# Kernel optimization log

Measured on AMD Instinct MI355X. Metric: run time of the kernel, lower is better.

## Reference

```python
import jax, jax.numpy as jnp
import numpy as np

N_NODES = 100_000
N_EDGES = 1_000_000
H = 128
NUM_STATES = 4
UPPER_T, LOWER_T, NUM_ITERS, TEMP_EVAL = 1.0, 0.1, 10000, 0.1


def temp_by_step(step, upper, lower, num_iters, temp_eval):
    # Python-level schedule: eval temp at step == -1, else linear anneal.
    if step == -1:
        return temp_eval
    frac = min(step / num_iters, 1.0)
    return upper + (lower - upper) * frac


def from_binary_states(states):
    # [*, k] bits -> integer id in [0, 2**k)
    weights = 2 ** jnp.arange(states.shape[-1])
    return (states * weights).sum(-1)


def setup_inputs() -> dict:
    key = jax.random.key(0)
    ks = jax.random.split(key, 20)
    N, E, h = N_NODES, N_EDGES, H
    node_states = jax.random.randint(ks[0], (N, NUM_STATES), 0, 2)
    edge_states = jax.random.randint(ks[1], (E, NUM_STATES), 0, 2)
    scalars = jax.random.normal(ks[2], (E, 1), jnp.float32)
    # first N edges are self-loops ordered by node id (required by the module's
    # node_scalars = scalars[src == dst] indexing convention)
    loops = jnp.arange(N)
    src = jax.random.randint(ks[3], (E - N,), 0, N)
    dst = jax.random.randint(ks[4], (E - N,), 0, N)
    dst = jnp.where(dst == src, (dst + 1) % N, dst)  # no accidental self-loops
    edge_index = jnp.stack([jnp.concatenate([loops, src]),
                            jnp.concatenate([loops, dst])])
    batched_reverse_idx = jax.random.randint(ks[5], (E,), 0, E)
    batch_scalars = jax.random.normal(ks[6], (E, 1, 1), jnp.float32)
    s = 0.02
    params = dict(
        node_emb=s * jax.random.normal(ks[7], (2 ** NUM_STATES, h), jnp.float32),
        edge_emb=s * jax.random.normal(ks[8], (2 ** NUM_STATES, h), jnp.float32),
        combine_W=s * jax.random.normal(ks[9], (2 * h, h), jnp.float32),
        combine_b=jnp.zeros((h,), jnp.float32),
        keep_W=s * jax.random.normal(ks[10], (h, 2), jnp.float32),
        keep_b=jnp.zeros((2,), jnp.float32),
        push_W=s * jax.random.normal(ks[11], (h, 2), jnp.float32),
        push_b=jnp.zeros((2,), jnp.float32),
        push_node_W=s * jax.random.normal(ks[12], (h, 2), jnp.float32),
        push_node_b=jnp.zeros((2,), jnp.float32),
        increment_W=s * jax.random.normal(ks[13], (h, 2), jnp.float32),
        increment_b=jnp.zeros((2,), jnp.float32),
    )
    return dict(node_states=node_states, edge_states=edge_states, scalars=scalars,
                edge_index=edge_index, batched_reverse_idx=batched_reverse_idx,
                batch_scalars=batch_scalars, processor_step=0, training_step=0,
                **params)


def reference(node_states, edge_states, scalars, edge_index, batched_reverse_idx,
              batch_scalars, processor_step, training_step,
              node_emb, edge_emb, combine_W, combine_b, keep_W, keep_b,
              push_W, push_b, push_node_W, push_node_b,
              increment_W, increment_b):
    N = node_states.shape[0]
    tau = temp_by_step(int(training_step), UPPER_T, LOWER_T, NUM_ITERS, TEMP_EVAL)
    # use_noise = config.use_noise (False) and training_step != -1 -> False

    node_fts = node_emb[from_binary_states(node_states)]   # [N, h]
    edge_fts = edge_emb[from_binary_states(edge_states)]   # [E, h]
    src, dst = edge_index[0], edge_index[1]
    fts = jnp.concatenate([edge_fts[batched_reverse_idx], node_fts[src]], axis=1)
    fts = fts @ combine_W + combine_b                       # [E, h]

    s = scalars.reshape(-1)                                 # [E]

    def pair_gumbel_first(W, b):
        # grouped (per-edge pair) softmax; take first component (== [::2])
        logits = (fts @ W + b) / tau                        # [E, 2]
        return jax.nn.softmax(logits, axis=-1)[:, 0]

    increment = 1.0 * pair_gumbel_first(increment_W, increment_b)
    keep = s * pair_gumbel_first(keep_W, keep_b)

    # push: first N edges are self-loops, self-loop of node i is edge i
    push_wo = pair_gumbel_first(push_W, push_b)
    push_w = pair_gumbel_first(push_node_W, push_node_b)
    node_scalars = s[:N]                                    # scalars at self-loops
    s_wo = s - node_scalars[dst]
    s_w = s_wo + node_scalars[src]
    acc = (jax.ops.segment_sum(push_wo * s_wo, dst, num_segments=N)
           + jax.ops.segment_sum(push_w * s_w, dst, num_segments=N))  # [N]
    edge_push = jnp.zeros_like(s).at[:N].set(acc)           # nonzero only on self-loops

    new_scalars = (increment + keep + edge_push)[:, None]   # [E, 1]
    target = batch_scalars[:, processor_step]               # [E, 1]
    loss = jnp.mean((target - new_scalars) ** 2)
    return new_scalars, loss
```

## Files before the change

kernel.cpp:

```cpp
#include <hip/hip_runtime.h>
#include <math.h>

#define N_NODES 100000
#define N_EDGES 1000000
#define HDIM 128
#define N_NONLOOP (N_EDGES - N_NODES)

typedef float  vfloat4 __attribute__((ext_vector_type(4)));

__device__ __forceinline__ float get_invtau(const int* __restrict__ training_step) {
    int step = training_step[0];
    float tau;
    if (step == -1) {
        tau = 0.1f;
    } else {
        float frac = fminf((float)step / 10000.0f, 1.0f);
        tau = 1.0f + (0.1f - 1.0f) * frac;
    }
    return 1.0f / tau;
}

__device__ __forceinline__ float wave_reduce(float v) {
    #pragma unroll
    for (int off = 32; off > 0; off >>= 1) v += __shfl_down(v, off, 64);
    return v;
}

__global__ __launch_bounds__(256) void precompute_tab1(
    const int* __restrict__ node_states,
    const float* __restrict__ s,
    const float* __restrict__ cW,
    const float* __restrict__ kW, const float* __restrict__ pW,
    const float* __restrict__ pnW, const float* __restrict__ iW,
    const int* __restrict__ tstep,
    float2* __restrict__ node_pack,
    float* __restrict__ acc,
    float* __restrict__ loss_out,
    float* __restrict__ uv)
{
    const int n = blockIdx.x * blockDim.x + threadIdx.x;
    if (n < N_NODES) {
        int4 st = ((const int4*)node_states)[n];
        const int idx = st.x + 2 * st.y + 4 * st.z + 8 * st.w;
        float2 np;
        np.x = s[n];
        np.y = __int_as_float(idx);
        node_pack[n] = np;
        acc[n] = 0.f;
    }
    if (n == 0) *loss_out = 0.f;

    if (blockIdx.x < 256) {
        __shared__ float wd[512];
        const float invtau = get_invtau(tstep);
        for (int i = threadIdx.x; i < 512; i += 256) {
            const int h = i >> 7, d = i & 127;
            const float* W = (h == 0) ? kW : (h == 1) ? pW : (h == 2) ? pnW : iW;
            wd[i] = W[2 * d] - W[2 * d + 1];
        }
        __syncthreads();

        const int row  = blockIdx.x * 4 + (threadIdx.x >> 6);
        const int lane = threadIdx.x & 63;
        const int half = row >> 9;
        const int r    = row & 511;
        const int h    = r >> 7, d = r & 127;
        const int cwrow = half * 128 + d;

        float p = cW[cwrow * 128 + lane]      * wd[h * 128 + lane]
                + cW[cwrow * 128 + 64 + lane] * wd[h * 128 + 64 + lane];
        p = wave_reduce(p);
        if (lane == 0) uv[row] = p * invtau;
    }
}

__global__ void tab_stage2(const float* __restrict__ node_emb,
                           const float* __restrict__ edge_emb,
                           const float* __restrict__ cb,
                           const float* __restrict__ kW, const float* __restrict__ kb,
                           const float* __restrict__ pW, const float* __restrict__ pb,
                           const float* __restrict__ pnW, const float* __restrict__ pnb,
                           const float* __restrict__ iW, const float* __restrict__ ib,
                           const int* __restrict__ tstep,
                           const float* __restrict__ uv,
                           float* __restrict__ tabs)
{
    const int w = blockIdx.x * 4 + (threadIdx.x >> 6);
    if (w >= 132) return;
    const int lane = threadIdx.x & 63;
    const float invtau = get_invtau(tstep);

    float p;
    if (w < 128) {
        const int isB = w >> 6, h = (w >> 4) & 3, i = w & 15;
        const float* emb = isB ? node_emb : edge_emb;
        const float* uvp = uv + isB * 512 + h * 128;
        p = emb[i * 128 + lane] * uvp[lane] + emb[i * 128 + 64 + lane] * uvp[64 + lane];
    } else {
        const int h = w - 128;
        const float* W = (h == 0) ? kW : (h == 1) ? pW : (h == 2) ? pnW : iW;
        p = cb[lane]      * (W[2 * lane] - W[2 * lane + 1])
          + cb[64 + lane] * (W[2 * (64 + lane)] - W[2 * (64 + lane) + 1]);
    }
    p = wave_reduce(p);
    if (lane == 0) {
        if (w < 64) {
            const int h = (w >> 4) & 3, i = w & 15;
            tabs[i * 4 + h] = p;
        } else if (w < 128) {
            const int h = (w >> 4) & 3, i = w & 15;
            tabs[64 + i * 4 + h] = p;
        } else {
            const int h = w - 128;
            const float* b = (h == 0) ? kb : (h == 1) ? pb : (h == 2) ? pnb : ib;
            tabs[128 + h] = (p + b[0] - b[1]) * invtau;
        }
    }
}

__global__ __launch_bounds__(256) void edge_kernel(
    const float* __restrict__ s,
    const int* __restrict__ src,
    const int* __restrict__ dst,
    const int* __restrict__ brev,
    const int* __restrict__ edge_states,
    const float2* __restrict__ node_pack,
    const float* __restrict__ tabs,
    const float* __restrict__ target,
    float* __restrict__ acc,
    float* __restrict__ out,
    float* __restrict__ loss_out)
{
    __shared__ float4 sf[33];
    if (threadIdx.x < 33) sf[threadIdx.x] = ((const float4*)tabs)[threadIdx.x];
    __syncthreads();

    const int t = blockIdx.x * blockDim.x + threadIdx.x;
    float lsum = 0.f;

    if (t < N_NONLOOP / 4) {
        const int g = (N_NODES / 4) + t;
        const int4   rv = ((const int4*)brev)[g];
        const int4   sr = ((const int4*)src)[g];
        const int4   ds = ((const int4*)dst)[g];
        const float4 sv = ((const float4*)s)[g];
        const vfloat4 tg = __builtin_nontemporal_load(&((const vfloat4*)target)[g]);

        const int rvv[4] = {rv.x, rv.y, rv.z, rv.w};
        const int srv[4] = {sr.x, sr.y, sr.z, sr.w};
        const int dsv[4] = {ds.x, ds.y, ds.z, ds.w};
        const float svv[4] = {sv.x, sv.y, sv.z, sv.w};
        const float tgv[4] = {tg.x, tg.y, tg.z, tg.w};

        int4  es[4];
        float2 np[4];
        float sd[4];
        #pragma unroll
        for (int j = 0; j < 4; ++j) {
            es[j] = ((const int4*)edge_states)[rvv[j]];
            np[j] = node_pack[srv[j]];
            sd[j] = node_pack[dsv[j]].x;
        }

        const float4 c4 = sf[32];
        float ov[4];
        #pragma unroll
        for (int j = 0; j < 4; ++j) {
            const int ei = es[j].x + 2 * es[j].y + 4 * es[j].z + 8 * es[j].w;
            const int   ni = __float_as_int(np[j].y);
            const float ss = np[j].x;
            const float4 a = sf[ei];
            const float4 b = sf[16 + ni];
            const float lk  = a.x + b.x + c4.x;
            const float lp  = a.y + b.y + c4.y;
            const float lpn = a.z + b.z + c4.z;
            const float li  = a.w + b.w + c4.w;
            const float pk  = 1.f / (1.f + __expf(-lk));
            const float pp  = 1.f / (1.f + __expf(-lp));
            const float ppn = 1.f / (1.f + __expf(-lpn));
            const float pi  = 1.f / (1.f + __expf(-li));

            const float s_wo = svv[j] - sd[j];
            const float s_w  = s_wo + ss;
            unsafeAtomicAdd(&acc[dsv[j]], pp * s_wo + ppn * s_w);

            ov[j] = pi + svv[j] * pk;
            const float d = tgv[j] - ov[j];
            lsum += d * d;
        }
        vfloat4 o4 = {ov[0], ov[1], ov[2], ov[3]};
        __builtin_nontemporal_store(o4, &((vfloat4*)out)[g]);
    }

    lsum = wave_reduce(lsum);
    __shared__ float wsum[4];
    const int lane = threadIdx.x & 63, wid = threadIdx.x >> 6;
    if (lane == 0) wsum[wid] = lsum;
    __syncthreads();
    if (threadIdx.x == 0) {
        const float tot = wsum[0] + wsum[1] + wsum[2] + wsum[3];
        atomicAdd(loss_out, tot * (1.0f / (float)N_EDGES));
    }
}

__global__ __launch_bounds__(256) void finalize_nodes(
    const int* __restrict__ brev,
    const int* __restrict__ edge_states,
    const float2* __restrict__ node_pack,
    const float* __restrict__ tabs,
    const float* __restrict__ target,
    const float* __restrict__ acc,
    float* __restrict__ out,
    float* __restrict__ loss_out)
{
    __shared__ float4 sf[33];
    if (threadIdx.x < 33) sf[threadIdx.x] = ((const float4*)tabs)[threadIdx.x];
    __syncthreads();

    const int n = blockIdx.x * blockDim.x + threadIdx.x;
    float sq = 0.f;
    if (n < N_NODES) {
        const int    rev = brev[n];
        const int4   est = ((const int4*)edge_states)[rev];
        const int    ei  = est.x + 2 * est.y + 4 * est.z + 8 * est.w;
        const float2 np  = node_pack[n];
        const int    ni  = __float_as_int(np.y);
        const float  sv  = np.x;

        const float4 a = sf[ei];
        const float4 b = sf[16 + ni];
        const float4 c4 = sf[32];
        const float lk  = a.x + b.x + c4.x;
        const float lpn = a.z + b.z + c4.z;
        const float li  = a.w + b.w + c4.w;
        const float pk  = 1.f / (1.f + __expf(-lk));
        const float ppn = 1.f / (1.f + __expf(-lpn));
        const float pi  = 1.f / (1.f + __expf(-li));

        const float v = pi + sv * (pk + ppn) + acc[n];
        out[n] = v;
        const float d = target[n] - v;
        sq = d * d;
    }
    sq = wave_reduce(sq);
    __shared__ float wsum[4];
    const int lane = threadIdx.x & 63, wid = threadIdx.x >> 6;
    if (lane == 0) wsum[wid] = sq;
    __syncthreads();
    if (threadIdx.x == 0) {
        const float tot = wsum[0] + wsum[1] + wsum[2] + wsum[3];
        atomicAdd(loss_out, tot * (1.0f / (float)N_EDGES));
    }
}

extern "C" void kernel_launch(void* const* d_in, const int* in_sizes, int n_in,
                              void* d_out, int out_size, void* d_ws, size_t ws_size,
                              hipStream_t stream) {
    const int*   node_states   = (const int*)d_in[0];
    const int*   edge_states   = (const int*)d_in[1];
    const float* scalars       = (const float*)d_in[2];
    const int*   edge_index    = (const int*)d_in[3];
    const int*   brev          = (const int*)d_in[4];
    const float* batch_scalars = (const float*)d_in[5];
    const int*   training_step = (const int*)d_in[7];
    const float* node_emb  = (const float*)d_in[8];
    const float* edge_emb  = (const float*)d_in[9];
    const float* combine_W = (const float*)d_in[10];
    const float* combine_b = (const float*)d_in[11];
    const float* keep_W  = (const float*)d_in[12];
    const float* keep_b  = (const float*)d_in[13];
    const float* push_W  = (const float*)d_in[14];
    const float* push_b  = (const float*)d_in[15];
    const float* pushn_W = (const float*)d_in[16];
    const float* pushn_b = (const float*)d_in[17];
    const float* inc_W   = (const float*)d_in[18];
    const float* inc_b   = (const float*)d_in[19];

    float* out = (float*)d_out;

    char* ws = (char*)d_ws;
    float*  tabs = (float*)ws;
    float*  uv   = (float*)(ws + 1024);
    float*  acc  = (float*)(ws + 1024 + 4096);
    float2* node_pack = (float2*)(ws + 1024 + 4096 + (size_t)N_NODES * 4);

    const int* srcp = edge_index;
    const int* dstp = edge_index + N_EDGES;

    precompute_tab1<<<(N_NODES + 255) / 256, 256, 0, stream>>>(
        node_states, scalars,
        combine_W, keep_W, push_W, pushn_W, inc_W, training_step,
        node_pack, acc, out + N_EDGES, uv);

    tab_stage2<<<33, 256, 0, stream>>>(node_emb, edge_emb, combine_b,
                                       keep_W, keep_b, push_W, push_b,
                                       pushn_W, pushn_b, inc_W, inc_b,
                                       training_step, uv, tabs);

    const int ethreads = N_NONLOOP / 4;
    edge_kernel<<<(ethreads + 255) / 256, 256, 0, stream>>>(
        scalars, srcp, dstp, brev, edge_states, node_pack, tabs, batch_scalars,
        acc, out, out + N_EDGES);

    finalize_nodes<<<(N_NODES + 255) / 256, 256, 0, stream>>>(
        brev, edge_states, node_pack, tabs, batch_scalars, acc, out, out + N_EDGES);
}
```

Before: 177.9 us.

## Precompute packed byte edge-state indices and fuse precompute kernels into one launch

```diff
diff --git a/kernel.cpp b/kernel.cpp
--- a/kernel.cpp
+++ b/kernel.cpp
@@ -1,5 +1,6 @@
 #include <hip/hip_runtime.h>
 #include <math.h>
+#include <stdint.h>
 
 #define N_NODES 100000
 #define N_EDGES 1000000
@@ -7,6 +8,7 @@
 #define N_NONLOOP (N_EDGES - N_NODES)
 
 typedef float  vfloat4 __attribute__((ext_vector_type(4)));
+typedef int    vint4   __attribute__((ext_vector_type(4)));
 
 __device__ __forceinline__ float get_invtau(const int* __restrict__ training_step) {
     int step = training_step[0];
@@ -26,95 +28,95 @@
     return v;
 }
 
-__global__ __launch_bounds__(256) void precompute_tab1(
+#define TAB_BLOCKS  33
+#define NODE_BLOCKS 391
+#define EI_BLOCKS   977
+
+__global__ __launch_bounds__(256) void fused_pre(
     const int* __restrict__ node_states,
     const float* __restrict__ s,
-    const float* __restrict__ cW,
-    const float* __restrict__ kW, const float* __restrict__ pW,
-    const float* __restrict__ pnW, const float* __restrict__ iW,
+    const int* __restrict__ edge_states,
+    const float* __restrict__ node_emb,
+    const float* __restrict__ edge_emb,
+    const float* __restrict__ cW, const float* __restrict__ cb,
+    const float* __restrict__ kW, const float* __restrict__ kb,
+    const float* __restrict__ pW, const float* __restrict__ pb,
+    const float* __restrict__ pnW, const float* __restrict__ pnb,
+    const float* __restrict__ iW, const float* __restrict__ ib,
     const int* __restrict__ tstep,
     float2* __restrict__ node_pack,
     float* __restrict__ acc,
-    float* __restrict__ loss_out,
-    float* __restrict__ uv)
+    uint8_t* __restrict__ ei,
+    float* __restrict__ tabs,
+    float* __restrict__ loss_out)
 {
-    const int n = blockIdx.x * blockDim.x + threadIdx.x;
-    if (n < N_NODES) {
-        int4 st = ((const int4*)node_states)[n];
-        const int idx = st.x + 2 * st.y + 4 * st.z + 8 * st.w;
-        float2 np;
-        np.x = s[n];
-        np.y = __int_as_float(idx);
-        node_pack[n] = np;
-        acc[n] = 0.f;
-    }
-    if (n == 0) *loss_out = 0.f;
-
-    if (blockIdx.x < 256) {
-        __shared__ float wd[512];
+    const int b = blockIdx.x;
+
+    if (b < TAB_BLOCKS) {
+        const int w    = b * 4 + (threadIdx.x >> 6);
+        const int lane = threadIdx.x & 63;
+        if (w >= 132) return;
         const float invtau = get_invtau(tstep);
-        for (int i = threadIdx.x; i < 512; i += 256) {
-            const int h = i >> 7, d = i & 127;
+
+        if (w < 128) {
+            const int isB = w >> 6, h = (w >> 4) & 3, i = w & 15;
+            const float* emb = isB ? node_emb : edge_emb;
+            const float* cWh = cW + isB * 128 * 128;
+            float t0 = 0.f, t1 = 0.f;
+            #pragma unroll 4
+            for (int l = 0; l < 128; ++l) {
+                const float el = emb[i * 128 + l];
+                t0 += el * cWh[l * 128 + lane];
+                t1 += el * cWh[l * 128 + 64 + lane];
+            }
             const float* W = (h == 0) ? kW : (h == 1) ? pW : (h == 2) ? pnW : iW;
-            wd[i] = W[2 * d] - W[2 * d + 1];
+            const float wd0 = W[2 * lane] - W[2 * lane + 1];
+            const float wd1 = W[2 * (lane + 64)] - W[2 * (lane + 64) + 1];
+            float p = t0 * wd0 + t1 * wd1;
+            p = wave_reduce(p);
+            if (lane == 0) tabs[isB * 64 + i * 4 + h] = p * invtau;
+        } else {
+            const int h = w & 3;
+            const float* W = (h == 0) ? kW : (h == 1) ? pW : (h == 2) ? pnW : iW;
+            const float wd0 = W[2 * lane] - W[2 * lane + 1];
+            const float wd1 = W[2 * (lane + 64)] - W[2 * (lane + 64) + 1];
+            float p = cb[lane] * wd0 + cb[64 + lane] * wd1;
+            p = wave_reduce(p);
+            if (lane == 0) {
+                const float* bb = (h == 0) ? kb : (h == 1) ? pb : (h == 2) ? pnb : ib;
+                tabs[128 + h] = (p + bb[0] - bb[1]) * invtau;
+            }
         }
-        __syncthreads();
-
-        const int row  = blockIdx.x * 4 + (threadIdx.x >> 6);
-        const int lane = threadIdx.x & 63;
-        const int half = row >> 9;
-        const int r    = row & 511;
-        const int h    = r >> 7, d = r & 127;
-        const int cwrow = half * 128 + d;
-
-        float p = cW[cwrow * 128 + lane]      * wd[h * 128 + lane]
-                + cW[cwrow * 128 + 64 + lane] * wd[h * 128 + 64 + lane];
-        p = wave_reduce(p);
-        if (lane == 0) uv[row] = p * invtau;
-    }
-}
-
-__global__ void tab_stage2(const float* __restrict__ node_emb,
-                           const float* __restrict__ edge_emb,
-                           const float* __restrict__ cb,
-                           const float* __restrict__ kW, const float* __restrict__ kb,
-                           const float* __restrict__ pW, const float* __restrict__ pb,
-                           const float* __restrict__ pnW, const float* __restrict__ pnb,
-                           const float* __restrict__ iW, const float* __restrict__ ib,
-                           const int* __restrict__ tstep,
-                           const float* __restrict__ uv,
-                           float* __restrict__ tabs)
-{
-    const int w = blockIdx.x * 4 + (threadIdx.x >> 6);
-    if (w >= 132) return;
-    const int lane = threadIdx.x & 63;
-    const float invtau = get_invtau(tstep);
-
-    float p;
-    if (w < 128) {
-        const int isB = w >> 6, h = (w >> 4) & 3, i = w & 15;
-        const float* emb = isB ? node_emb : edge_emb;
-        const float* uvp = uv + isB * 512 + h * 128;
-        p = emb[i * 128 + lane] * uvp[lane] + emb[i * 128 + 64 + lane] * uvp[64 + lane];
-    } else {
-        const int h = w - 128;
-        const float* W = (h == 0) ? kW : (h == 1) ? pW : (h == 2) ? pnW : iW;
-        p = cb[lane]      * (W[2 * lane] - W[2 * lane + 1])
-          + cb[64 + lane] * (W[2 * (64 + lane)] - W[2 * (64 + lane) + 1]);
-    }
-    p = wave_reduce(p);
-    if (lane == 0) {
-        if (w < 64) {
-            const int h = (w >> 4) & 3, i = w & 15;
-            tabs[i * 4 + h] = p;
-        } else if (w < 128) {
-            const int h = (w >> 4) & 3, i = w & 15;
-            tabs[64 + i * 4 + h] = p;
-        } else {
-            const int h = w - 128;
-            const float* b = (h == 0) ? kb : (h == 1) ? pb : (h == 2) ? pnb : ib;
-            tabs[128 + h] = (p + b[0] - b[1]) * invtau;
+        return;
+    }
+
+    if (b < TAB_BLOCKS + NODE_BLOCKS) {
+        const int n = (b - TAB_BLOCKS) * 256 + threadIdx.x;
+        if (n == 0) *loss_out = 0.f;
+        if (n < N_NODES) {
+            vint4 st = __builtin_nontemporal_load(&((const vint4*)node_states)[n]);
+            const int idx = st.x + 2 * st.y + 4 * st.z + 8 * st.w;
+            float2 np;
+            np.x = s[n];
+            np.y = __int_as_float(idx);
+            node_pack[n] = np;
+            acc[n] = 0.f;
         }
+        return;
+    }
+
+    const int t = (b - TAB_BLOCKS - NODE_BLOCKS) * 256 + threadIdx.x;
+    if (t < N_EDGES / 4) {
+        const vint4* esp = (const vint4*)edge_states + 4 * t;
+        vint4 e0 = __builtin_nontemporal_load(esp + 0);
+        vint4 e1 = __builtin_nontemporal_load(esp + 1);
+        vint4 e2 = __builtin_nontemporal_load(esp + 2);
+        vint4 e3 = __builtin_nontemporal_load(esp + 3);
+        const uint32_t i0 = e0.x + 2 * e0.y + 4 * e0.z + 8 * e0.w;
+        const uint32_t i1 = e1.x + 2 * e1.y + 4 * e1.z + 8 * e1.w;
+        const uint32_t i2 = e2.x + 2 * e2.y + 4 * e2.z + 8 * e2.w;
+        const uint32_t i3 = e3.x + 2 * e3.y + 4 * e3.z + 8 * e3.w;
+        ((uint32_t*)ei)[t] = i0 | (i1 << 8) | (i2 << 16) | (i3 << 24);
     }
 }
 
@@ -123,7 +125,7 @@
     const int* __restrict__ src,
     const int* __restrict__ dst,
     const int* __restrict__ brev,
-    const int* __restrict__ edge_states,
+    const uint8_t* __restrict__ ei,
     const float2* __restrict__ node_pack,
     const float* __restrict__ tabs,
     const float* __restrict__ target,
@@ -136,40 +138,42 @@
     __syncthreads();
 
     const int t = blockIdx.x * blockDim.x + threadIdx.x;
+    const bool active = (t < N_NONLOOP / 4);
     float lsum = 0.f;
-
-    if (t < N_NONLOOP / 4) {
-        const int g = (N_NODES / 4) + t;
-        const int4   rv = ((const int4*)brev)[g];
-        const int4   sr = ((const int4*)src)[g];
-        const int4   ds = ((const int4*)dst)[g];
-        const float4 sv = ((const float4*)s)[g];
+    float ov[4], av[4];
+    int   dsv[4];
+    int   g = 0;
+
+    if (active) {
+        g = (N_NODES / 4) + t;
+        const vint4   rv = __builtin_nontemporal_load(&((const vint4*)brev)[g]);
+        const vint4   sr = __builtin_nontemporal_load(&((const vint4*)src)[g]);
+        const vint4   ds = __builtin_nontemporal_load(&((const vint4*)dst)[g]);
+        const vfloat4 sv = __builtin_nontemporal_load(&((const vfloat4*)s)[g]);
         const vfloat4 tg = __builtin_nontemporal_load(&((const vfloat4*)target)[g]);
 
         const int rvv[4] = {rv.x, rv.y, rv.z, rv.w};
         const int srv[4] = {sr.x, sr.y, sr.z, sr.w};
-        const int dsv[4] = {ds.x, ds.y, ds.z, ds.w};
+        dsv[0] = ds.x; dsv[1] = ds.y; dsv[2] = ds.z; dsv[3] = ds.w;
         const float svv[4] = {sv.x, sv.y, sv.z, sv.w};
         const float tgv[4] = {tg.x, tg.y, tg.z, tg.w};
 
-        int4  es[4];
+        int    eidx[4];
         float2 np[4];
-        float sd[4];
+        float  sd[4];
         #pragma unroll
         for (int j = 0; j < 4; ++j) {
-            es[j] = ((const int4*)edge_states)[rvv[j]];
-            np[j] = node_pack[srv[j]];
-            sd[j] = node_pack[dsv[j]].x;
+            eidx[j] = ei[rvv[j]];
+            np[j]   = node_pack[srv[j]];
+            sd[j]   = node_pack[dsv[j]].x;
         }
 
         const float4 c4 = sf[32];
-        float ov[4];
         #pragma unroll
         for (int j = 0; j < 4; ++j) {
-            const int ei = es[j].x + 2 * es[j].y + 4 * es[j].z + 8 * es[j].w;
             const int   ni = __float_as_int(np[j].y);
             const float ss = np[j].x;
-            const float4 a = sf[ei];
+            const float4 a = sf[eidx[j]];
             const float4 b = sf[16 + ni];
             const float lk  = a.x + b.x + c4.x;
             const float lp  = a.y + b.y + c4.y;
@@ -182,14 +186,12 @@
 
             const float s_wo = svv[j] - sd[j];
             const float s_w  = s_wo + ss;
-            unsafeAtomicAdd(&acc[dsv[j]], pp * s_wo + ppn * s_w);
+            av[j] = pp * s_wo + ppn * s_w;
 
             ov[j] = pi + svv[j] * pk;
             const float d = tgv[j] - ov[j];
             lsum += d * d;
         }
-        vfloat4 o4 = {ov[0], ov[1], ov[2], ov[3]};
-        __builtin_nontemporal_store(o4, &((vfloat4*)out)[g]);
     }
 
     lsum = wave_reduce(lsum);
@@ -201,11 +203,19 @@
         const float tot = wsum[0] + wsum[1] + wsum[2] + wsum[3];
         atomicAdd(loss_out, tot * (1.0f / (float)N_EDGES));
     }
+
+    if (active) {
+        #pragma unroll
+        for (int j = 0; j < 4; ++j)
+            unsafeAtomicAdd(&acc[dsv[j]], av[j]);
+        vfloat4 o4 = {ov[0], ov[1], ov[2], ov[3]};
+        __builtin_nontemporal_store(o4, &((vfloat4*)out)[g]);
+    }
 }
 
 __global__ __launch_bounds__(256) void finalize_nodes(
     const int* __restrict__ brev,
-    const int* __restrict__ edge_states,
+    const uint8_t* __restrict__ ei,
     const float2* __restrict__ node_pack,
     const float* __restrict__ tabs,
     const float* __restrict__ target,
@@ -218,17 +228,17 @@
     __syncthreads();
 
     const int n = blockIdx.x * blockDim.x + threadIdx.x;
-    float sq = 0.f;
-    if (n < N_NODES) {
+    const bool active = (n < N_NODES);
+    float sq = 0.f, v = 0.f;
+    if (active) {
         const int    rev = brev[n];
-        const int4   est = ((const int4*)edge_states)[rev];
-        const int    ei  = est.x + 2 * est.y + 4 * est.z + 8 * est.w;
+        const int    eidx = ei[rev];
         const float2 np  = node_pack[n];
         const int    ni  = __float_as_int(np.y);
         const float  sv  = np.x;
 
-        const float4 a = sf[ei];
-        const float4 b = sf[16 + ni];
+        const float4 a  = sf[eidx];
+        const float4 b  = sf[16 + ni];
         const float4 c4 = sf[32];
         const float lk  = a.x + b.x + c4.x;
         const float lpn = a.z + b.z + c4.z;
@@ -237,8 +247,7 @@
         const float ppn = 1.f / (1.f + __expf(-lpn));
         const float pi  = 1.f / (1.f + __expf(-li));
 
-        const float v = pi + sv * (pk + ppn) + acc[n];
-        out[n] = v;
+        v = pi + sv * (pk + ppn) + acc[n];
         const float d = target[n] - v;
         sq = d * d;
     }
@@ -251,6 +260,7 @@
         const float tot = wsum[0] + wsum[1] + wsum[2] + wsum[3];
         atomicAdd(loss_out, tot * (1.0f / (float)N_EDGES));
     }
+    if (active) out[n] = v;
 }
 
 extern "C" void kernel_launch(void* const* d_in, const int* in_sizes, int n_in,
@@ -279,29 +289,25 @@
     float* out = (float*)d_out;
 
     char* ws = (char*)d_ws;
-    float*  tabs = (float*)ws;
-    float*  uv   = (float*)(ws + 1024);
-    float*  acc  = (float*)(ws + 1024 + 4096);
-    float2* node_pack = (float2*)(ws + 1024 + 4096 + (size_t)N_NODES * 4);
+    float*   tabs      = (float*)ws;
+    float*   acc       = (float*)(ws + 1024);
+    float2*  node_pack = (float2*)(ws + 1024 + (size_t)N_NODES * 4);
+    uint8_t* ei        = (uint8_t*)(ws + 1024 + (size_t)N_NODES * 12);
 
     const int* srcp = edge_index;
     const int* dstp = edge_index + N_EDGES;
 
-    precompute_tab1<<<(N_NODES + 255) / 256, 256, 0, stream>>>(
-        node_states, scalars,
-        combine_W, keep_W, push_W, pushn_W, inc_W, training_step,
-        node_pack, acc, out + N_EDGES, uv);
-
-    tab_stage2<<<33, 256, 0, stream>>>(node_emb, edge_emb, combine_b,
-                                       keep_W, keep_b, push_W, push_b,
-                                       pushn_W, pushn_b, inc_W, inc_b,
-                                       training_step, uv, tabs);
+    fused_pre<<<TAB_BLOCKS + NODE_BLOCKS + EI_BLOCKS, 256, 0, stream>>>(
+        node_states, scalars, edge_states, node_emb, edge_emb,
+        combine_W, combine_b, keep_W, keep_b, push_W, push_b,
+        pushn_W, pushn_b, inc_W, inc_b, training_step,
+        node_pack, acc, ei, tabs, out + N_EDGES);
 
     const int ethreads = N_NONLOOP / 4;
     edge_kernel<<<(ethreads + 255) / 256, 256, 0, stream>>>(
-        scalars, srcp, dstp, brev, edge_states, node_pack, tabs, batch_scalars,
+        scalars, srcp, dstp, brev, ei, node_pack, tabs, batch_scalars,
         acc, out, out + N_EDGES);
 
     finalize_nodes<<<(N_NODES + 255) / 256, 256, 0, stream>>>(
-        brev, edge_states, node_pack, tabs, batch_scalars, acc, out, out + N_EDGES);
-}
+        brev, ei, node_pack, tabs, batch_scalars, acc, out, out + N_EDGES);
+}
```

Result: slower. 187.4 us (+5.3%).
